# Kernel optimization log

Measured on AMD Instinct MI355X. Metric: run time of the kernel, lower is better.

## Reference

```python
import jax, jax.numpy as jnp
import numpy as np

NUM_HEADS = 8
NUM_GROUPS = 32
EPS = 1e-5


def setup_inputs() -> dict:
    key = jax.random.key(0)
    ks = jax.random.split(key, 6)
    C = 512
    scale = 1.0 / np.sqrt(C)
    return {
        "q": jax.random.normal(ks[0], (2, C, 64, 64), dtype=jnp.float32),
        "gn_w": jnp.ones((C,), jnp.float32),
        "gn_b": jnp.zeros((C,), jnp.float32),
        "wq": jax.random.normal(ks[1], (C, C), jnp.float32) * scale,
        "bq": jnp.zeros((C,), jnp.float32),
        "wk": jax.random.normal(ks[2], (C, C), jnp.float32) * scale,
        "bk": jnp.zeros((C,), jnp.float32),
        "wv": jax.random.normal(ks[3], (C, C), jnp.float32) * scale,
        "bv": jnp.zeros((C,), jnp.float32),
        "wo": jax.random.normal(ks[4], (C, C), jnp.float32) * scale,
        "bo": jnp.zeros((C,), jnp.float32),
    }


def _group_norm(x, w, b):
    # x: [B, C, H, W]
    B, C, H, W = x.shape
    xg = x.reshape(B, NUM_GROUPS, C // NUM_GROUPS, H, W)
    mean = xg.mean(axis=(2, 3, 4), keepdims=True)
    var = xg.var(axis=(2, 3, 4), keepdims=True)
    xn = ((xg - mean) * jax.lax.rsqrt(var + EPS)).reshape(B, C, H, W)
    return xn * w[None, :, None, None] + b[None, :, None, None]


def reference(q, gn_w, gn_b, wq, bq, wk, bk, wv, bv, wo, bo):
    B, C, H, W = q.shape
    hd = C // NUM_HEADS
    resid = q
    x = _group_norm(q, gn_w, gn_b)
    x = x.reshape(B, C, H * W).transpose(0, 2, 1)  # [B, N, C]
    # torch Linear: y = x @ W.T + b  (self-attention: k = v = x)
    qp = x @ wq.T + bq
    kp = x @ wk.T + bk
    vp = x @ wv.T + bv
    N = H * W
    def split(t):  # [B, N, C] -> [B, h, N, hd]
        return t.reshape(B, N, NUM_HEADS, hd).transpose(0, 2, 1, 3)
    qh, kh, vh = split(qp), split(kp), split(vp)
    scores = jnp.einsum('bhnc,bhmc->bhnm', qh, kh) / jnp.sqrt(jnp.float32(hd))
    attn = jax.nn.softmax(scores, axis=-1)
    out = jnp.einsum('bhnm,bhmc->bhnc', attn, vh)
    out = out.transpose(0, 2, 1, 3).reshape(B, N, C)
    out = out @ wo.T + bo
    out2d = out.transpose(0, 2, 1).reshape(B, C, H, W)
    return out2d + resid
```

## Files before the change

### kernel.cpp

```cpp
#include <hip/hip_runtime.h>
#include <hip/hip_bf16.h>
#include <cstdint>
#include <cstddef>

using bf16x8   = __attribute__((ext_vector_type(8))) short;
using f32x4    = __attribute__((ext_vector_type(4))) float;
using f32x16   = __attribute__((ext_vector_type(16))) float;
using ushort8  = __attribute__((ext_vector_type(8))) unsigned short;
using ushort4v = __attribute__((ext_vector_type(4))) unsigned short;
using float4v  = __attribute__((ext_vector_type(4))) float;
using float2v  = __attribute__((ext_vector_type(2))) float;

#define MFMA16(a,b,c) __builtin_amdgcn_mfma_f32_16x16x32_bf16((a),(b),(c),0,0,0)
#define MFMA32(a,b,c) __builtin_amdgcn_mfma_f32_32x32x16_bf16((a),(b),(c),0,0,0)

#define QSCALE 0.18033688011112042f

__device__ __forceinline__ unsigned short f2bf(float f){
    union { float f; unsigned u; } v; v.f = f;
    unsigned r = v.u + 0x7FFFu + ((v.u >> 16) & 1u);
    return (unsigned short)(r >> 16);
}

__device__ __forceinline__ int cvtpk(float lo, float hi){
    int r;
    asm volatile("v_cvt_pk_bf16_f32 %0, %1, %2" : "=v"(r) : "v"(lo), "v"(hi));
    return r;
}

#if __has_builtin(__builtin_amdgcn_permlane32_swap)
__device__ __forceinline__ void plswap(int &a, int &b){
    auto r = __builtin_amdgcn_permlane32_swap(a, b, false, false);
    a = r[0]; b = r[1];
}
#else
__device__ __forceinline__ void plswap(int &a, int &b){
    int ta = __shfl_xor(a, 32), tb = __shfl_xor(b, 32);
    bool hi = ((threadIdx.x & 63) >= 32);
    int na = hi ? tb : a;
    int nb = hi ? b  : ta;
    a = na; b = nb;
}
#endif

__device__ __forceinline__ void gload16(const unsigned short* g, unsigned short* l){
    __builtin_amdgcn_global_load_lds(
        (const __attribute__((address_space(1))) void*)g,
        (__attribute__((address_space(3))) void*)l,
        16, 0, 0);
}

__global__ __launch_bounds__(256) void gn_stats_wconv(const float* __restrict__ x,
                                                      float2v* __restrict__ parts,
                                                      const float* __restrict__ w0, const float* __restrict__ w1,
                                                      const float* __restrict__ w2, const float* __restrict__ w3,
                                                      unsigned short* wqk, unsigned short* wv, unsigned short* wo){
    int bid = blockIdx.x;
    if (bid < 512){
        const float4v* p4 = (const float4v*)(x + (size_t)bid * 8192);
        float s = 0.f, ss = 0.f;
        #pragma unroll
        for (int i = 0; i < 8; i++){
            float4v v = p4[i*256 + threadIdx.x];
            s  += v[0]+v[1]+v[2]+v[3];
            ss += v[0]*v[0]+v[1]*v[1]+v[2]*v[2]+v[3]*v[3];
        }
        __shared__ float ls[4], lss[4];
        int lane = threadIdx.x & 63, w = threadIdx.x >> 6;
        #pragma unroll
        for (int o = 32; o > 0; o >>= 1){ s += __shfl_down(s, o); ss += __shfl_down(ss, o); }
        if (lane == 0){ ls[w] = s; lss[w] = ss; }
        __syncthreads();
        if (threadIdx.x == 0){
            float2v p;
            p[0] = ls[0]+ls[1]+ls[2]+ls[3];
            p[1] = lss[0]+lss[1]+lss[2]+lss[3];
            parts[bid] = p;
        }
    } else {
        int i2 = bid - 512;
        int y = i2 >> 8, bx = i2 & 255;
        const float* src; unsigned short* dst; float sc = 1.0f;
        switch (y){
            case 0: src = w0; dst = wqk;          sc = QSCALE; break;
            case 1: src = w1; dst = wqk + 512*512; break;
            case 2: src = w2; dst = wv; break;
            default: src = w3; dst = wo; break;
        }
        int i = (bx*256 + threadIdx.x) * 4;
        float4v v = *(const float4v*)(src + i);
        ushort4v o;
        #pragma unroll
        for (int j = 0; j < 4; j++) o[j] = f2bf(v[j]*sc);
        *(ushort4v*)(dst + i) = o;
    }
}

__global__ __launch_bounds__(256) void gn_apply(const float* __restrict__ x,
                                                const float2v* __restrict__ parts,
                                                const float* __restrict__ gw,
                                                const float* __restrict__ gb,
                                                unsigned short* __restrict__ xn){
    int b = blockIdx.z, c0 = blockIdx.y * 64, n0 = blockIdx.x * 64;
    __shared__ unsigned short tile[64][68];
    __shared__ float gmean[4], grstd[4];
    if (threadIdx.x < 4){
        int g = b*32 + (c0 >> 4) + threadIdx.x;
        float s = 0.f, ss = 0.f;
        #pragma unroll
        for (int e = 0; e < 8; e++){
            float2v p = parts[g*8 + e];
            s += p[0]; ss += p[1];
        }
        float m = s * (1.f/65536.f);
        float var = ss * (1.f/65536.f) - m*m;
        gmean[threadIdx.x] = m;
        grstd[threadIdx.x] = rsqrtf(var + 1e-5f);
    }
    __syncthreads();
    for (int i = threadIdx.x; i < 64*16; i += 256){
        int row = i >> 4, f4 = i & 15;
        int c = c0 + row;
        int gl = row >> 4;
        float rs = grstd[gl];
        float wgt = gw[c] * rs;
        float bia = gb[c] - gmean[gl] * wgt;
        float4v v = *(const float4v*)(x + ((size_t)(b*512 + c))*4096 + n0 + f4*4);
        ushort4v o;
        #pragma unroll
        for (int j = 0; j < 4; j++) o[j] = f2bf(v[j]*wgt + bia);
        *(ushort4v*)&tile[row][f4*4] = o;
    }
    __syncthreads();
    for (int i = threadIdx.x; i < 64*8; i += 256){
        int nr = i >> 3, c8 = i & 7;
        ushort8 o;
        #pragma unroll
        for (int j = 0; j < 8; j++) o[j] = tile[c8*8 + j][nr];
        *(ushort8*)(xn + ((size_t)(b*4096 + n0 + nr))*512 + c0 + c8*8) = o;
    }
}

__global__ __launch_bounds__(256) void gemm_qkv(const unsigned short* __restrict__ xn,
                                                const unsigned short* __restrict__ wqk,
                                                const unsigned short* __restrict__ Wv,
                                                const float* __restrict__ bq,
                                                const float* __restrict__ bk,
                                                const float* __restrict__ bv,
                                                unsigned short* __restrict__ Q,
                                                unsigned short* __restrict__ K,
                                                unsigned short* __restrict__ Vt){
    __shared__ unsigned short Al[128*32];
    __shared__ unsigned short Bl[128*32];
    int bid = blockIdx.x;
    int t = threadIdx.x, lane = t & 63, w = t >> 6;
    int wr = w >> 1, wc = w & 1;
    int lr = lane >> 2, lc = lane & 3;

    if (bid < 512){
        int m0 = (bid & 63) * 128, n0 = (bid >> 6) * 128;
        f32x4 acc[4][4] = {};
        const unsigned short* Asrc = xn  + (size_t)(m0 + w*32 + lr)*512 + lc*8;
        const unsigned short* Bsrc = wqk + (size_t)(n0 + w*32 + lr)*512 + lc*8;
        unsigned short* Adst = &Al[(w*32)*32];
        unsigned short* Bdst = &Bl[(w*32)*32];

        for (int ks = 0; ks < 16; ks++){
            gload16(Asrc + ks*32,          Adst);
            gload16(Asrc + ks*32 + 16*512, Adst + 16*32);
            gload16(Bsrc + ks*32,          Bdst);
            gload16(Bsrc + ks*32 + 16*512, Bdst + 16*32);
            asm volatile("s_waitcnt vmcnt(0)" ::: "memory");
            __syncthreads();
            bf16x8 a[4], b[4];
            #pragma unroll
            for (int mi = 0; mi < 4; mi++) a[mi] = *(bf16x8*)&Al[(wr*64 + mi*16 + (lane&15))*32 + (lane>>4)*8];
            #pragma unroll
            for (int ni = 0; ni < 4; ni++) b[ni] = *(bf16x8*)&Bl[(wc*64 + ni*16 + (lane&15))*32 + (lane>>4)*8];
            #pragma unroll
            for (int mi = 0; mi < 4; mi++)
                #pragma unroll
                for (int ni = 0; ni < 4; ni++)
                    acc[mi][ni] = MFMA16(a[mi], b[ni], acc[mi][ni]);
            __syncthreads();
        }

        int cK = n0 >> 9;
        const float* bias = cK ? bk : bq;
        unsigned short* dst0 = cK ? K : Q;
        float bsc = cK ? 1.0f : QSCALE;
        #pragma unroll
        for (int mi = 0; mi < 4; mi++)
            #pragma unroll
            for (int ni = 0; ni < 4; ni++)
                #pragma unroll
                for (int r = 0; r < 4; r++){
                    int mrow = m0 + wr*64 + mi*16 + (lane>>4)*4 + r;
                    int col  = (n0 & 511) + wc*64 + ni*16 + (lane&15);
                    int b_ = mrow >> 12, n = mrow & 4095;
                    int h = col >> 6, d = col & 63;
                    float v = acc[mi][ni][r] + bias[col]*bsc;
                    dst0[(size_t)((b_*8+h)*4096 + n)*64 + d] = f2bf(v);
                }
    } else {
        int i2 = bid - 512;
        int m0 = (i2 >> 6) * 64, n0 = (i2 & 63) * 128;
        f32x4 acc[2][4] = {};
        const unsigned short* Asrc = Wv + (size_t)(m0 + w*16 + lr)*512 + lc*8;
        const unsigned short* Bsrc = xn + (size_t)(n0 + w*32 + lr)*512 + lc*8;
        unsigned short* Adst = &Al[(w*16)*32];
        unsigned short* Bdst = &Bl[(w*32)*32];

        for (int ks = 0; ks < 16; ks++){
            gload16(Asrc + ks*32,          Adst);
            gload16(Bsrc + ks*32,          Bdst);
            gload16(Bsrc + ks*32 + 16*512, Bdst + 16*32);
            asm volatile("s_waitcnt vmcnt(0)" ::: "memory");
            __syncthreads();
            bf16x8 a[2], b[4];
            #pragma unroll
            for (int mi = 0; mi < 2; mi++) a[mi] = *(bf16x8*)&Al[(wr*32 + mi*16 + (lane&15))*32 + (lane>>4)*8];
            #pragma unroll
            for (int ni = 0; ni < 4; ni++) b[ni] = *(bf16x8*)&Bl[(wc*64 + ni*16 + (lane&15))*32 + (lane>>4)*8];
            #pragma unroll
            for (int mi = 0; mi < 2; mi++)
                #pragma unroll
                for (int ni = 0; ni < 4; ni++)
                    acc[mi][ni] = MFMA16(a[mi], b[ni], acc[mi][ni]);
            __syncthreads();
        }
        #pragma unroll
        for (int mi = 0; mi < 2; mi++)
            #pragma unroll
            for (int ni = 0; ni < 4; ni++)
                #pragma unroll
                for (int r = 0; r < 4; r++){
                    int row  = m0 + wr*32 + mi*16 + (lane>>4)*4 + r;
                    int colm = n0 + wc*64 + ni*16 + (lane&15);
                    int b_ = colm >> 12, n = colm & 4095;
                    int h = row >> 6, d = row & 63;
                    float v = acc[mi][ni][r] + bv[row];
                    Vt[(size_t)((b_*8+h)*64 + d)*4096 + n] = f2bf(v);
                }
    }
}

__global__ __launch_bounds__(256) void gemm_o2(const unsigned short* __restrict__ Wo,
                                               const unsigned short* __restrict__ Om,
                                               const float* __restrict__ bo,
                                               const float* __restrict__ resid,
                                               float* __restrict__ outp){
    __shared__ unsigned short Al[64*32];
    __shared__ unsigned short Bl[128*32];
    int t = threadIdx.x, lane = t & 63, w = t >> 6;
    int wr = w >> 1, wc = w & 1;
    int m0 = blockIdx.y * 64, n0 = blockIdx.x * 128;
    int lr = lane >> 2, lc = lane & 3;
    f32x4 acc[2][4] = {};

    const unsigned short* Asrc = Wo + (size_t)(m0 + w*16 + lr)*512 + lc*8;
    const unsigned short* Bsrc = Om + (size_t)(n0 + w*32 + lr)*512 + lc*8;
    unsigned short* Adst = &Al[(w*16)*32];
    unsigned short* Bdst = &Bl[(w*32)*32];

    for (int ks = 0; ks < 16; ks++){
        gload16(Asrc + ks*32,          Adst);
        gload16(Bsrc + ks*32,          Bdst);
        gload16(Bsrc + ks*32 + 16*512, Bdst + 16*32);
        asm volatile("s_waitcnt vmcnt(0)" ::: "memory");
        __syncthreads();
        bf16x8 a[2], b[4];
        #pragma unroll
        for (int mi = 0; mi < 2; mi++) a[mi] = *(bf16x8*)&Al[(wr*32 + mi*16 + (lane&15))*32 + (lane>>4)*8];
        #pragma unroll
        for (int ni = 0; ni < 4; ni++) b[ni] = *(bf16x8*)&Bl[(wc*64 + ni*16 + (lane&15))*32 + (lane>>4)*8];
        #pragma unroll
        for (int mi = 0; mi < 2; mi++)
            #pragma unroll
            for (int ni = 0; ni < 4; ni++)
                acc[mi][ni] = MFMA16(a[mi], b[ni], acc[mi][ni]);
        __syncthreads();
    }
    #pragma unroll
    for (int mi = 0; mi < 2; mi++)
        #pragma unroll
        for (int ni = 0; ni < 4; ni++)
            #pragma unroll
            for (int r = 0; r < 4; r++){
                int row  = m0 + wr*32 + mi*16 + (lane>>4)*4 + r;
                int colm = n0 + wc*64 + ni*16 + (lane&15);
                int b_ = colm >> 12, n = colm & 4095;
                size_t oi = ((size_t)(b_*512 + row))*4096 + n;
                outp[oi] = acc[mi][ni][r] + bo[row] + resid[oi];
            }
}

__global__ __launch_bounds__(128, 2) void attn5(const unsigned short* __restrict__ Q,
                                                const unsigned short* __restrict__ K,
                                                const unsigned short* __restrict__ Vt,
                                                unsigned short* __restrict__ O){
    int bid = blockIdx.x;
    int idx = bid >> 3;
    int bh = ((bid & 7) << 1) | (idx >> 6);
    int qt = idx & 63;
    int t = threadIdx.x, lane = t & 63, w = t >> 6;
    int ln = lane & 31, hi = lane >> 5;
    int q0 = qt * 64;

    __shared__ unsigned short Kl[2][64*64];
    __shared__ unsigned short Vl[2][64*64];

    const unsigned short* Qb = Q  + (size_t)bh * 4096 * 64;
    const unsigned short* Kb = K  + (size_t)bh * 4096 * 64;
    const unsigned short* Vb = Vt + (size_t)bh * 64 * 4096;

    bf16x8 bqa[4], bqb[4];
    #pragma unroll
    for (int dsub = 0; dsub < 4; dsub++){
        bqa[dsub] = *(const bf16x8*)(Qb + (size_t)(q0 + ln)*64      + dsub*16 + hi*8);
        bqb[dsub] = *(const bf16x8*)(Qb + (size_t)(q0 + 32 + ln)*64 + dsub*16 + hi*8);
    }

    int srow = lane >> 3;
    int sswz = (lane & 7) ^ srow;

    auto stage = [&](int buf, int kt){
        int kv0 = kt * 64;
        #pragma unroll
        for (int i = 0; i < 4; i++){
            int r0 = w*32 + i*8;
            gload16(Kb + (size_t)(kv0 + r0 + srow)*64 + sswz*8, &Kl[buf][r0*64]);
        }
        #pragma unroll
        for (int i = 0; i < 4; i++){
            int r0 = w*32 + i*8;
            gload16(Vb + (size_t)(r0 + srow)*4096 + kv0 + sswz*8, &Vl[buf][r0*64]);
        }
    };

    stage(0, 0);

    f32x16 o0a, o1a, o0b, o1b, z;
    #pragma unroll
    for (int r = 0; r < 16; r++){ o0a[r]=0.f; o1a[r]=0.f; o0b[r]=0.f; o1b[r]=0.f; z[r]=0.f; }
    float lsA = 0.f, lsB = 0.f;

    const char* KbA = (const char*)&Kl[0][0] + (w*32 + ln)*128;
    const char* VbA = (const char*)&Vl[0][0] + ln*128;
    int swzr = (ln & 7) << 4;

    for (int kt = 0; kt < 64; kt++){
        asm volatile("s_waitcnt vmcnt(0)" ::: "memory");
        __builtin_amdgcn_s_barrier();
        __builtin_amdgcn_sched_barrier(0);
        if (kt < 63) stage((kt + 1) & 1, kt + 1);
        __builtin_amdgcn_sched_barrier(0);

        int boff = (kt & 1) * (64*64*2);

        f32x16 sA, sB;
        {
            int cb = (hi*16) ^ swzr;
            bf16x8 ak = *(const bf16x8*)(KbA + boff + cb);
            sA = MFMA32(ak, bqa[0], z);
            sB = MFMA32(ak, bqb[0], z);
        }
        __builtin_amdgcn_s_setprio(1);
        #pragma unroll
        for (int dsub = 1; dsub < 4; dsub++){
            int cb = (dsub*32 + hi*16) ^ swzr;
            bf16x8 ak = *(const bf16x8*)(KbA + boff + cb);
            sA = MFMA32(ak, bqa[dsub], sA);
            sB = MFMA32(ak, bqb[dsub], sB);
        }
        __builtin_amdgcn_s_setprio(0);

        #pragma unroll
        for (int r = 0; r < 16; r++){ sA[r] = __builtin_amdgcn_exp2f(sA[r]); lsA += sA[r]; }
        #pragma unroll
        for (int r = 0; r < 16; r++){ sB[r] = __builtin_amdgcn_exp2f(sB[r]); lsB += sB[r]; }

        __builtin_amdgcn_s_setprio(1);
        #pragma unroll
        for (int hsel = 0; hsel < 2; hsel++){
            int obp = hsel * 8;
            int a0 = cvtpk(sA[obp+0], sA[obp+1]);
            int a1 = cvtpk(sA[obp+2], sA[obp+3]);
            int c0 = cvtpk(sA[obp+4], sA[obp+5]);
            int c1 = cvtpk(sA[obp+6], sA[obp+7]);
            plswap(a0, c0);
            plswap(a1, c1);
            union { int i[4]; bf16x8 v; } fuA;
            fuA.i[0] = a0; fuA.i[1] = a1; fuA.i[2] = c0; fuA.i[3] = c1;

            int d0 = cvtpk(sB[obp+0], sB[obp+1]);
            int d1 = cvtpk(sB[obp+2], sB[obp+3]);
            int e0 = cvtpk(sB[obp+4], sB[obp+5]);
            int e1 = cvtpk(sB[obp+6], sB[obp+7]);
            plswap(d0, e0);
            plswap(d1, e1);
            union { int i[4]; bf16x8 v; } fuB;
            fuB.i[0] = d0; fuB.i[1] = d1; fuB.i[2] = e0; fuB.i[3] = e1;

            int cb = ((w*4 + hsel*2 + hi) << 4) ^ swzr;
            bf16x8 av0 = *(const bf16x8*)(VbA + boff + cb);
            bf16x8 av1 = *(const bf16x8*)(VbA + boff + 32*128 + cb);
            o0a = MFMA32(av0, fuA.v, o0a);
            o1a = MFMA32(av1, fuA.v, o1a);
            o0b = MFMA32(av0, fuB.v, o0b);
            o1b = MFMA32(av1, fuB.v, o1b);
        }
        __builtin_amdgcn_s_setprio(0);
    }

    lsA += __shfl_xor(lsA, 32);
    lsB += __shfl_xor(lsB, 32);
    __syncthreads();
    float* m1 = (float*)&Kl[0][0];
    float* m2 = (float*)&Vl[0][0];
    if (w == 1){
        #pragma unroll
        for (int r = 0; r < 16; r++){
            m1[r*64 + lane]        = o0a[r];
            m1[1024 + r*64 + lane] = o1a[r];
            m2[r*64 + lane]        = o0b[r];
            m2[1024 + r*64 + lane] = o1b[r];
        }
        if (hi == 0){ m2[2048 + ln] = lsA; m2[2048 + 32 + ln] = lsB; }
    }
    __syncthreads();
    if (w == 0){
        #pragma unroll
        for (int r = 0; r < 16; r++){
            o0a[r] += m1[r*64 + lane];
            o1a[r] += m1[1024 + r*64 + lane];
            o0b[r] += m2[r*64 + lane];
            o1b[r] += m2[1024 + r*64 + lane];
        }
        float rA = 1.0f / (lsA + m2[2048 + ln]);
        float rB = 1.0f / (lsB + m2[2048 + 32 + ln]);
        int b = bh >> 3, h = bh & 7;
        unsigned short* dstA = O + (size_t)(b*4096 + q0 + ln)*512      + h*64;
        unsigned short* dstB = O + (size_t)(b*4096 + q0 + 32 + ln)*512 + h*64;
        #pragma unroll
        for (int m = 0; m < 2; m++){
            const f32x16& ovA = m ? o1a : o0a;
            const f32x16& ovB = m ? o1b : o0b;
            #pragma unroll
            for (int g = 0; g < 4; g++){
                int d = m*32 + g*8 + hi*4;
                ushort4v pkA, pkB;
                #pragma unroll
                for (int j = 0; j < 4; j++){
                    pkA[j] = f2bf(ovA[g*4 + j] * rA);
                    pkB[j] = f2bf(ovB[g*4 + j] * rB);
                }
                *(ushort4v*)(dstA + d) = pkA;
                *(ushort4v*)(dstB + d) = pkB;
            }
        }
    }
}

extern "C" void kernel_launch(void* const* d_in, const int* in_sizes, int n_in,
                              void* d_out, int out_size, void* d_ws, size_t ws_size,
                              hipStream_t stream) {
    const float* q    = (const float*)d_in[0];
    const float* gn_w = (const float*)d_in[1];
    const float* gn_b = (const float*)d_in[2];
    const float* wq   = (const float*)d_in[3];
    const float* bq   = (const float*)d_in[4];
    const float* wk   = (const float*)d_in[5];
    const float* bk   = (const float*)d_in[6];
    const float* wv   = (const float*)d_in[7];
    const float* bv   = (const float*)d_in[8];
    const float* wo   = (const float*)d_in[9];
    const float* bo   = (const float*)d_in[10];
    float* outp = (float*)d_out;

    char* ws = (char*)d_ws;
    float2v* parts = (float2v*)ws;
    unsigned short* xn  = (unsigned short*)(ws + 8192);
    const size_t TOK = (size_t)8192 * 512;
    unsigned short* wqkb = xn + TOK;
    unsigned short* wvb  = wqkb + 1024*512;
    unsigned short* wob  = wvb + 512*512;
    unsigned short* Qb   = wob + 512*512;
    unsigned short* Kb   = Qb + TOK;
    unsigned short* Vt   = Kb + TOK;
    unsigned short* Ob   = Vt + TOK;

    gn_stats_wconv<<<1536, 256, 0, stream>>>(q, parts, wq, wk, wv, wo, wqkb, wvb, wob);
    gn_apply<<<dim3(64, 8, 2), 256, 0, stream>>>(q, parts, gn_w, gn_b, xn);
    gemm_qkv<<<1024, 256, 0, stream>>>(xn, wqkb, wvb, bq, bk, bv, Qb, Kb, Vt);
    attn5<<<1024, 128, 0, stream>>>(Qb, Kb, Vt, Ob);
    gemm_o2<<<dim3(64, 8), 256, 0, stream>>>(wob, Ob, bo, q, outp);
}
```

Measured before the change: 135.1 us.

## Make attention staging wave-private and prefetch two tiles ahead without barriers

Each wave now stages only the K rows and the V columns it consumes itself, with a new swizzled layout for its private V slice. That removes the per-iteration workgroup barrier. Loads are issued two tiles ahead: the prefetch runs after the compute of the current tile, and the wait is relaxed to vmcnt(8) so one tile's loads stay in flight. The aim is to take barrier stalls and exposed global-load latency out of the attention main loop. The risk is an ordering hazard between LDS reads and the asynchronous LDS writes into the reused buffer.

After: 134.2 us, median of 2. About the same (-0.7%).

```diff
diff --git a/kernel.cpp b/kernel.cpp
--- a/kernel.cpp
+++ b/kernel.cpp
@@ -295,7 +295,7 @@
             }
 }
 
-__global__ __launch_bounds__(128, 2) void attn5(const unsigned short* __restrict__ Q,
+__global__ __launch_bounds__(128, 2) void attn9(const unsigned short* __restrict__ Q,
                                                 const unsigned short* __restrict__ K,
                                                 const unsigned short* __restrict__ Vt,
                                                 unsigned short* __restrict__ O){
@@ -308,7 +308,7 @@
     int q0 = qt * 64;
 
     __shared__ unsigned short Kl[2][64*64];
-    __shared__ unsigned short Vl[2][64*64];
+    __shared__ unsigned short Vl[2][2][64*32];
 
     const unsigned short* Qb = Q  + (size_t)bh * 4096 * 64;
     const unsigned short* Kb = K  + (size_t)bh * 4096 * 64;
@@ -323,22 +323,25 @@
 
     int srow = lane >> 3;
     int sswz = (lane & 7) ^ srow;
-
-    auto stage = [&](int buf, int kt){
+    int vdl = lane >> 2;
+    int vsl = (lane & 3) ^ ((vdl >> 1) & 3);
+
+    auto stage = [&](int kt){
         int kv0 = kt * 64;
+        unsigned short* kdst = &Kl[kt & 1][0];
         #pragma unroll
         for (int i = 0; i < 4; i++){
             int r0 = w*32 + i*8;
-            gload16(Kb + (size_t)(kv0 + r0 + srow)*64 + sswz*8, &Kl[buf][r0*64]);
-        }
-        #pragma unroll
-        for (int i = 0; i < 4; i++){
-            int r0 = w*32 + i*8;
-            gload16(Vb + (size_t)(r0 + srow)*4096 + kv0 + sswz*8, &Vl[buf][r0*64]);
-        }
+            gload16(Kb + (size_t)(kv0 + r0 + srow)*64 + sswz*8, kdst + r0*64);
+        }
+        unsigned short* vdst = &Vl[kt & 1][w][0];
+        #pragma unroll
+        for (int i = 0; i < 4; i++)
+            gload16(Vb + (size_t)(i*16 + vdl)*4096 + kv0 + w*32 + vsl*8, vdst + i*512);
     };
 
-    stage(0, 0);
+    stage(0);
+    stage(1);
 
     f32x16 o0a, o1a, o0b, o1b, z;
     #pragma unroll
@@ -346,22 +349,22 @@
     float lsA = 0.f, lsB = 0.f;
 
     const char* KbA = (const char*)&Kl[0][0] + (w*32 + ln)*128;
-    const char* VbA = (const char*)&Vl[0][0] + ln*128;
     int swzr = (ln & 7) << 4;
+    const char* VbW = (const char*)&Vl[0][w][0];
+    int vrswz = (ln >> 1) & 3;
 
     for (int kt = 0; kt < 64; kt++){
-        asm volatile("s_waitcnt vmcnt(0)" ::: "memory");
-        __builtin_amdgcn_s_barrier();
+        if (kt < 63) asm volatile("s_waitcnt vmcnt(8)" ::: "memory");
+        else         asm volatile("s_waitcnt vmcnt(0)" ::: "memory");
         __builtin_amdgcn_sched_barrier(0);
-        if (kt < 63) stage((kt + 1) & 1, kt + 1);
-        __builtin_amdgcn_sched_barrier(0);
-
-        int boff = (kt & 1) * (64*64*2);
+
+        int kboff = (kt & 1) * (64*64*2);
+        int vboff = (kt & 1) * (2*64*32*2);
 
         f32x16 sA, sB;
         {
             int cb = (hi*16) ^ swzr;
-            bf16x8 ak = *(const bf16x8*)(KbA + boff + cb);
+            bf16x8 ak = *(const bf16x8*)(KbA + kboff + cb);
             sA = MFMA32(ak, bqa[0], z);
             sB = MFMA32(ak, bqb[0], z);
         }
@@ -369,7 +372,7 @@
         #pragma unroll
         for (int dsub = 1; dsub < 4; dsub++){
             int cb = (dsub*32 + hi*16) ^ swzr;
-            bf16x8 ak = *(const bf16x8*)(KbA + boff + cb);
+            bf16x8 ak = *(const bf16x8*)(KbA + kboff + cb);
             sA = MFMA32(ak, bqa[dsub], sA);
             sB = MFMA32(ak, bqb[dsub], sB);
         }
@@ -402,22 +405,26 @@
             union { int i[4]; bf16x8 v; } fuB;
             fuB.i[0] = d0; fuB.i[1] = d1; fuB.i[2] = e0; fuB.i[3] = e1;
 
-            int cb = ((w*4 + hsel*2 + hi) << 4) ^ swzr;
-            bf16x8 av0 = *(const bf16x8*)(VbA + boff + cb);
-            bf16x8 av1 = *(const bf16x8*)(VbA + boff + 32*128 + cb);
+            int p0 = (((hsel*2 + hi) ^ vrswz) << 4);
+            bf16x8 av0 = *(const bf16x8*)(VbW + vboff + ln*64 + p0);
+            bf16x8 av1 = *(const bf16x8*)(VbW + vboff + (32 + ln)*64 + p0);
             o0a = MFMA32(av0, fuA.v, o0a);
             o1a = MFMA32(av1, fuA.v, o1a);
             o0b = MFMA32(av0, fuB.v, o0b);
             o1b = MFMA32(av1, fuB.v, o1b);
         }
         __builtin_amdgcn_s_setprio(0);
+
+        __builtin_amdgcn_sched_barrier(0);
+        if (kt < 62) stage(kt + 2);
+        __builtin_amdgcn_sched_barrier(0);
     }
 
     lsA += __shfl_xor(lsA, 32);
     lsB += __shfl_xor(lsB, 32);
     __syncthreads();
     float* m1 = (float*)&Kl[0][0];
-    float* m2 = (float*)&Vl[0][0];
+    float* m2 = (float*)&Vl[0][0][0];
     if (w == 1){
         #pragma unroll
         for (int r = 0; r < 16; r++){
@@ -493,6 +500,6 @@
     gn_stats_wconv<<<1536, 256, 0, stream>>>(q, parts, wq, wk, wv, wo, wqkb, wvb, wob);
     gn_apply<<<dim3(64, 8, 2), 256, 0, stream>>>(q, parts, gn_w, gn_b, xn);
     gemm_qkv<<<1024, 256, 0, stream>>>(xn, wqkb, wvb, bq, bk, bv, Qb, Kb, Vt);
-    attn5<<<1024, 128, 0, stream>>>(Qb, Kb, Vt, Ob);
+    attn9<<<1024, 128, 0, stream>>>(Qb, Kb, Vt, Ob);
     gemm_o2<<<dim3(64, 8), 256, 0, stream>>>(wob, Ob, bo, q, outp);
 }
```
